# Optimization experiments

Hardware: AMD Instinct MI355X
Metric: run time of the kernel (lower is better)

The kernel has to match this reference:

```python
import jax, jax.numpy as jnp
import numpy as np

B, S, D, H = 2, 2048, 2048, 16
HD = D // H  # 128


def _rope(t, cos, sin):
    # t: [B, S, H, HD]; cos/sin: [S, HD//2]
    te, to = t[..., ::2], t[..., 1::2]
    c = cos[None, :, None, :]
    s = sin[None, :, None, :]
    re = te * c - to * s
    im = te * s + to * c
    # interleave back (matches tf.stack(..., axis=-1) + reshape)
    return jnp.stack([re, im], axis=-1).reshape(t.shape)


def setup_inputs() -> dict:
    key = jax.random.key(0)
    ks = jax.random.split(key, 6)
    x = jax.random.normal(ks[0], (B, S, D), dtype=jnp.float32)
    Wq = jax.random.normal(ks[1], (D, D), dtype=jnp.float32) * 0.02
    Wk = jax.random.normal(ks[2], (D, D), dtype=jnp.float32) * 0.02
    Wv = jax.random.normal(ks[3], (D, D), dtype=jnp.float32) * 0.02
    Wo = jax.random.normal(ks[4], (D, D), dtype=jnp.float32) * 0.02
    # rotary embeddings: freqs_cis = exp(i * pos * inv_freq)
    inv_freq = 1.0 / (10000.0 ** (jnp.arange(0, HD, 2, dtype=jnp.float32) / HD))  # [HD//2]
    angles = jnp.arange(S, dtype=jnp.float32)[:, None] * inv_freq[None, :]  # [S, HD//2]
    freqs_cos = jnp.cos(angles)
    freqs_sin = jnp.sin(angles)
    # additive causal mask [1,1,S,S]
    causal = jnp.tril(jnp.ones((S, S), dtype=bool))
    mask = jnp.where(causal, 0.0, -1e9).astype(jnp.float32)[None, None]
    return {"x": x, "Wq": Wq, "Wk": Wk, "Wv": Wv, "Wo": Wo,
            "freqs_cos": freqs_cos, "freqs_sin": freqs_sin, "mask": mask}


def reference(x, Wq, Wk, Wv, Wo, freqs_cos, freqs_sin, mask):
    b, s, d = x.shape
    xq = (x @ Wq).reshape(b, s, H, HD)
    xk = (x @ Wk).reshape(b, s, H, HD)
    xv = (x @ Wv).reshape(b, s, H, HD)
    xq = _rope(xq, freqs_cos, freqs_sin)
    xk = _rope(xk, freqs_cos, freqs_sin)
    # [B, H, S, HD]
    xq = xq.transpose(0, 2, 1, 3)
    xk = xk.transpose(0, 2, 1, 3)
    xv = xv.transpose(0, 2, 1, 3)
    scores = jnp.einsum('bhqd,bhkd->bhqk', xq, xk) / jnp.sqrt(jnp.float32(HD))
    scores = scores + mask[:, :, :s, :s]
    probs = jax.nn.softmax(scores + 1e-9, axis=-1)
    out = jnp.einsum('bhqk,bhkd->bhqd', probs, xv)
    out = out.transpose(0, 2, 1, 3).reshape(b, s, d)
    return out @ Wo
```

## Files before the change

kernel.cpp:

```cpp
#include <hip/hip_runtime.h>
#include <cstdint>

#define BB 2
#define SS 2048
#define DD 2048
#define HH 16
#define HDIM 128
#define MM (BB * SS)

typedef __attribute__((ext_vector_type(8))) short bf16x8;
typedef __attribute__((ext_vector_type(4))) short bf16x4;
typedef __attribute__((ext_vector_type(4))) float f32x4;
typedef __attribute__((ext_vector_type(16))) float f32x16;

__device__ inline short f2bf(float f) {
  union { float f; unsigned u; } v; v.f = f;
  unsigned r = v.u + 0x7FFFu + ((v.u >> 16) & 1u);
  return (short)(r >> 16);
}
__device__ inline float bf2f(short s) {
  union { float f; unsigned u; } v;
  v.u = ((unsigned)(unsigned short)s) << 16;
  return v.f;
}
__device__ inline float asf(int u) { union { int i; float f; } v; v.i = u; return v.f; }
__device__ inline int asi(float f) { union { float f; int i; } v; v.f = f; return v.i; }

__device__ inline unsigned cvtpk_bf16(float lo, float hi) {
  unsigned r;
  asm("v_cvt_pk_bf16_f32 %0, %1, %2" : "=v"(r) : "v"(lo), "v"(hi));
  return r;
}

__device__ inline void gll16(const void* g, void* l) {
  __builtin_amdgcn_global_load_lds(
      (const __attribute__((address_space(1))) void*)g,
      (__attribute__((address_space(3))) void*)l, 16, 0, 0);
}

__global__ __launch_bounds__(256) void cast_bf16_kernel(
    const float* __restrict__ x, short* __restrict__ y, int n4) {
  int i = blockIdx.x * 256 + threadIdx.x;
  if (i >= n4) return;
  float4 v = reinterpret_cast<const float4*>(x)[i];
  bf16x4 o;
  o[0] = f2bf(v.x); o[1] = f2bf(v.y); o[2] = f2bf(v.z); o[3] = f2bf(v.w);
  reinterpret_cast<bf16x4*>(y)[i] = o;
}

__global__ __launch_bounds__(256) void transpose_cast_kernel(
    const float* __restrict__ W, short* __restrict__ Wt) {
  __shared__ short tile[64][65];
  int c = threadIdx.x & 63, r4 = threadIdx.x >> 6;
  int n0 = blockIdx.x << 6, k0 = blockIdx.y << 6;
#pragma unroll
  for (int p = 0; p < 16; ++p) {
    int r = (p << 2) + r4;
    tile[c][r] = f2bf(W[(size_t)(k0 + r) * DD + n0 + c]);
  }
  __syncthreads();
#pragma unroll
  for (int p = 0; p < 16; ++p) {
    int r = (p << 2) + r4;
    Wt[(size_t)(n0 + r) * DD + k0 + c] = tile[r][c];
  }
}

__global__ __launch_bounds__(256) void qkv_gemm_kernel(
    const short* __restrict__ A, const short* __restrict__ Bt,
    short* __restrict__ Qb, short* __restrict__ Kb, short* __restrict__ Vt,
    const float* __restrict__ fc, const float* __restrict__ fs) {
  __shared__ short smem[128 * 136];
  short* As = smem;
  short* Bs = smem + 8192;
  const int tid = threadIdx.x;
  const int lane = tid & 63, w = tid >> 6;
  const int cl = lane & 15, gq = lane >> 4;
  const int wm = w >> 1, wn = w & 1;
  const int m0 = blockIdx.y << 7, n0 = blockIdx.x << 7;
  const int mat = n0 >> 11;
  f32x4 acc[4][4];
#pragma unroll
  for (int i = 0; i < 4; ++i)
#pragma unroll
    for (int j = 0; j < 4; ++j) {
      f32x4 z = {0.f, 0.f, 0.f, 0.f};
      acc[i][j] = z;
    }
  const int lrow = lane >> 3;
  const int lseg = (lane & 7) ^ lrow;

  for (int k0 = 0; k0 < DD; k0 += 64) {
#pragma unroll
    for (int i = 0; i < 4; ++i) {
      int r0 = ((w << 2) + i) << 3;
      gll16(&A[(size_t)(m0 + r0 + lrow) * DD + k0 + (lseg << 3)], &As[r0 << 6]);
      gll16(&Bt[(size_t)(n0 + r0 + lrow) * DD + k0 + (lseg << 3)], &Bs[r0 << 6]);
    }
    __syncthreads();
#pragma unroll
    for (int ks = 0; ks < 2; ++ks) {
      bf16x8 af[4], bfr[4];
#pragma unroll
      for (int f = 0; f < 4; ++f) {
        int ra = (wm << 6) + (f << 4) + cl;
        af[f] = *reinterpret_cast<const bf16x8*>(
            &As[((ra << 6) + (ks << 5) + (gq << 3)) ^ ((ra & 7) << 3)]);
        int rb = (wn << 6) + (f << 4) + cl;
        bfr[f] = *reinterpret_cast<const bf16x8*>(
            &Bs[((rb << 6) + (ks << 5) + (gq << 3)) ^ ((rb & 7) << 3)]);
      }
#pragma unroll
      for (int fm = 0; fm < 4; ++fm)
#pragma unroll
        for (int fn = 0; fn < 4; ++fn)
          acc[fm][fn] = __builtin_amdgcn_mfma_f32_16x16x32_bf16(
              af[fm], bfr[fn], acc[fm][fn], 0, 0, 0);
    }
    __syncthreads();
  }

  if (mat < 2) {
    const float qs = (mat == 0) ? 0.127517448f : 1.0f;
    short* Dst = (mat == 0) ? Qb : Kb;
#pragma unroll
    for (int fm = 0; fm < 4; ++fm)
#pragma unroll
      for (int r = 0; r < 4; ++r) {
        int mrow = m0 + (wm << 6) + (fm << 4) + (gq << 2) + r;
        int s = mrow & (SS - 1);
#pragma unroll
        for (int fn = 0; fn < 4; ++fn) {
          int c = (wn << 6) + (fn << 4) + cl;
          int i = c >> 1;
          float cv = fc[s * 64 + i], sv = fs[s * 64 + i];
          float v = acc[fm][fn][r];
          float vp = __shfl_xor(v, 1, 64);
          float out = (c & 1) ? (v * cv + vp * sv) : (v * cv - vp * sv);
          Dst[(size_t)mrow * DD + ((n0 + c) & (DD - 1))] = f2bf(out * qs);
        }
      }
  } else {
    short* Tt = smem;
#pragma unroll
    for (int fm = 0; fm < 4; ++fm)
#pragma unroll
      for (int fn = 0; fn < 4; ++fn) {
        int c = (wn << 6) + (fn << 4) + cl;
        int rb = (wm << 6) + (fm << 4) + (gq << 2);
        bf16x4 v4;
#pragma unroll
        for (int rr = 0; rr < 4; ++rr) v4[rr] = f2bf(acc[fm][fn][rr]);
        *reinterpret_cast<bf16x4*>(&Tt[c * 136 + rb]) = v4;
      }
    __syncthreads();
    int d = tid >> 1, half = tid & 1;
    int bq = m0 >> 11, s0loc = m0 & (SS - 1);
    int hv = (n0 >> 7) - 32;
    size_t vb = (((size_t)(bq * 16 + hv) * HDIM + d) * SS) + s0loc + half * 64;
#pragma unroll
    for (int j = 0; j < 8; ++j) {
      bf16x8 v = *reinterpret_cast<const bf16x8*>(&Tt[d * 136 + half * 64 + j * 8]);
      *reinterpret_cast<bf16x8*>(&Vt[vb + j * 8]) = v;
    }
  }
}

__global__ __launch_bounds__(256) void gemm_kernel(
    const short* __restrict__ A, const short* __restrict__ Bt, float* __restrict__ C,
    int Mdim, int Ndim, int Kdim) {
  __shared__ short As[128 * 64];
  __shared__ short Bs[128 * 64];
  int tid = threadIdx.x;
  int lane = tid & 63, w = tid >> 6;
  int cl = lane & 15, gq = lane >> 4;
  int wm = w >> 1, wn = w & 1;
  int m0 = blockIdx.y << 7, n0 = blockIdx.x << 7;
  f32x4 acc[4][4];
#pragma unroll
  for (int i = 0; i < 4; ++i)
#pragma unroll
    for (int j = 0; j < 4; ++j) {
      f32x4 z = {0.f, 0.f, 0.f, 0.f};
      acc[i][j] = z;
    }
  int lrow = lane >> 3;
  int lseg = (lane & 7) ^ lrow;

  for (int k0 = 0; k0 < Kdim; k0 += 64) {
#pragma unroll
    for (int i = 0; i < 4; ++i) {
      int r0 = ((w << 2) + i) << 3;
      gll16(&A[(size_t)(m0 + r0 + lrow) * Kdim + k0 + (lseg << 3)], &As[r0 << 6]);
      gll16(&Bt[(size_t)(n0 + r0 + lrow) * Kdim + k0 + (lseg << 3)], &Bs[r0 << 6]);
    }
    __syncthreads();
#pragma unroll
    for (int ks = 0; ks < 2; ++ks) {
      bf16x8 af[4], bfr[4];
#pragma unroll
      for (int f = 0; f < 4; ++f) {
        int ra = (wm << 6) + (f << 4) + cl;
        af[f] = *reinterpret_cast<const bf16x8*>(
            &As[((ra << 6) + (ks << 5) + (gq << 3)) ^ ((ra & 7) << 3)]);
        int rb = (wn << 6) + (f << 4) + cl;
        bfr[f] = *reinterpret_cast<const bf16x8*>(
            &Bs[((rb << 6) + (ks << 5) + (gq << 3)) ^ ((rb & 7) << 3)]);
      }
#pragma unroll
      for (int fm = 0; fm < 4; ++fm)
#pragma unroll
        for (int fn = 0; fn < 4; ++fn)
          acc[fm][fn] = __builtin_amdgcn_mfma_f32_16x16x32_bf16(
              af[fm], bfr[fn], acc[fm][fn], 0, 0, 0);
    }
    __syncthreads();
  }
#pragma unroll
  for (int fm = 0; fm < 4; ++fm)
#pragma unroll
    for (int r = 0; r < 4; ++r) {
      int mrow = m0 + (wm << 6) + (fm << 4) + (gq << 2) + r;
#pragma unroll
      for (int fn = 0; fn < 4; ++fn) {
        int ncol = n0 + (wn << 6) + (fn << 4) + cl;
        C[(size_t)mrow * Ndim + ncol] = acc[fm][fn][r];
      }
    }
}

__global__ __launch_bounds__(256, 2) void attn_kernel(
    const short* __restrict__ Q, const short* __restrict__ K,
    const short* __restrict__ Vt, short* __restrict__ O) {
  __shared__ short Kl[2][64 * 128];
  __shared__ short Vl[2][128 * 64];
  const int id = blockIdx.x;
  const int qi = 15 - (id >> 5);
  const int bh = id & 31;
  const int b = bh >> 4, h = bh & 15;
  const int tid = threadIdx.x;
  const int lane = tid & 63, w = tid >> 6;
  const int l31 = lane & 31, hi = lane >> 5;
  const int qw = qi * 128 + w * 32;
  const int qg = qw + l31;

  const short* Kbase = K + (size_t)b * SS * DD + h * HDIM;
  const short* Vbase = Vt + (size_t)bh * HDIM * SS;
  int krow[4], kq[4], vd[4], vs[4];
#pragma unroll
  for (int i = 0; i < 4; ++i) {
    int c = w * 4 + i;
    krow[i] = c * 4 + (lane >> 4);
    kq[i] = (lane & 15) ^ (krow[i] & 7);
    vd[i] = c * 8 + (lane >> 3);
    vs[i] = (lane & 7) ^ (vd[i] & 7);
  }

  bf16x8 qf[8];
  const size_t qoff = ((size_t)b * SS + qg) * DD + h * HDIM;
#pragma unroll
  for (int s = 0; s < 8; ++s)
    qf[s] = *reinterpret_cast<const bf16x8*>(&Q[qoff + s * 16 + hi * 8]);

  f32x16 ot[4];
#pragma unroll
  for (int dt = 0; dt < 4; ++dt)
#pragma unroll
    for (int r = 0; r < 16; ++r) ot[dt][r] = 0.f;
  float m_run = -INFINITY, l_run = 0.f;

  const int NT = 2 * qi + 2;

#pragma unroll
  for (int i = 0; i < 4; ++i) {
    gll16(Kbase + (size_t)krow[i] * DD + kq[i] * 8, &Kl[0][(w * 4 + i) * 512]);
    gll16(Vbase + (size_t)vd[i] * SS + vs[i] * 8, &Vl[0][(w * 4 + i) * 512]);
  }
  __syncthreads();

  for (int t = 0; t < NT; ++t) {
    const int cur = t & 1;
    if (t + 1 < NT) {
      const int nt64 = (t + 1) * 64;
#pragma unroll
      for (int i = 0; i < 4; ++i) {
        gll16(Kbase + (size_t)(nt64 + krow[i]) * DD + kq[i] * 8,
              &Kl[cur ^ 1][(w * 4 + i) * 512]);
        gll16(Vbase + (size_t)vd[i] * SS + nt64 + vs[i] * 8,
              &Vl[cur ^ 1][(w * 4 + i) * 512]);
      }
    }

    if (t * 64 <= qw + 31) {
      const short* Kc = Kl[cur];
      const short* Vc = Vl[cur];
      f32x16 st0, st1;
#pragma unroll
      for (int r = 0; r < 16; ++r) { st0[r] = 0.f; st1[r] = 0.f; }
      __builtin_amdgcn_s_setprio(1);
#pragma unroll
      for (int s = 0; s < 8; ++s) {
        const int cs = (s * 2 + hi);
        bf16x8 kf0 = *reinterpret_cast<const bf16x8*>(
            &Kc[l31 * 128 + ((cs ^ (l31 & 7)) << 3)]);
        st0 = __builtin_amdgcn_mfma_f32_32x32x16_bf16(kf0, qf[s], st0, 0, 0, 0);
        bf16x8 kf1 = *reinterpret_cast<const bf16x8*>(
            &Kc[(32 + l31) * 128 + ((cs ^ (l31 & 7)) << 3)]);
        st1 = __builtin_amdgcn_mfma_f32_32x32x16_bf16(kf1, qf[s], st1, 0, 0, 0);
      }
      __builtin_amdgcn_s_setprio(0);
      if (t * 64 + 63 > qw) {
#pragma unroll
        for (int r = 0; r < 16; ++r) {
          int dl = (r & 3) + 8 * (r >> 2) + 4 * hi;
          if (t * 64 + dl > qg) st0[r] = -1e30f;
          if (t * 64 + 32 + dl > qg) st1[r] = -1e30f;
        }
      }
      float mx[16];
#pragma unroll
      for (int r = 0; r < 16; ++r) mx[r] = fmaxf(st0[r], st1[r]);
#pragma unroll
      for (int off = 8; off >= 1; off >>= 1)
#pragma unroll
        for (int r = 0; r < 8; ++r)
          if (r < off) mx[r] = fmaxf(mx[r], mx[r + off]);
      float pm = mx[0];
      {
        auto sw = __builtin_amdgcn_permlane32_swap(asi(pm), asi(pm), false, false);
        pm = fmaxf(asf(sw[0]), asf(sw[1]));
      }
      if (!__all(pm <= m_run + 11.5f)) {
        float mn = fmaxf(m_run, pm);
        float al = exp2f(m_run - mn);
        m_run = mn;
        l_run *= al;
#pragma unroll
        for (int dt = 0; dt < 4; ++dt)
#pragma unroll
          for (int r = 0; r < 16; ++r) ot[dt][r] *= al;
      }
#pragma unroll
      for (int r = 0; r < 16; ++r) st0[r] = exp2f(st0[r] - m_run);
#pragma unroll
      for (int r = 0; r < 16; ++r) st1[r] = exp2f(st1[r] - m_run);
      float sm[16];
#pragma unroll
      for (int r = 0; r < 16; ++r) sm[r] = st0[r] + st1[r];
#pragma unroll
      for (int off = 8; off >= 1; off >>= 1)
#pragma unroll
        for (int r = 0; r < 8; ++r)
          if (r < off) sm[r] += sm[r + off];
      float ps = sm[0];
      {
        auto sw = __builtin_amdgcn_permlane32_swap(asi(ps), asi(ps), false, false);
        ps = asf(sw[0]) + asf(sw[1]);
      }
      l_run += ps;

      bf16x8 pf[4];
#pragma unroll
      for (int s = 0; s < 4; ++s) {
        float e0, e1, e2, e3, e4, e5, e6, e7;
        if (s < 2) {
          e0 = st0[8 * s + 0]; e1 = st0[8 * s + 1]; e2 = st0[8 * s + 2]; e3 = st0[8 * s + 3];
          e4 = st0[8 * s + 4]; e5 = st0[8 * s + 5]; e6 = st0[8 * s + 6]; e7 = st0[8 * s + 7];
        } else {
          e0 = st1[8 * (s - 2) + 0]; e1 = st1[8 * (s - 2) + 1]; e2 = st1[8 * (s - 2) + 2]; e3 = st1[8 * (s - 2) + 3];
          e4 = st1[8 * (s - 2) + 4]; e5 = st1[8 * (s - 2) + 5]; e6 = st1[8 * (s - 2) + 6]; e7 = st1[8 * (s - 2) + 7];
        }
        unsigned a0 = cvtpk_bf16(e0, e1);
        unsigned a1 = cvtpk_bf16(e2, e3);
        unsigned b0 = cvtpk_bf16(e4, e5);
        unsigned b1 = cvtpk_bf16(e6, e7);
        auto r0 = __builtin_amdgcn_permlane32_swap((int)a0, (int)b0, false, false);
        auto r1 = __builtin_amdgcn_permlane32_swap((int)a1, (int)b1, false, false);
        union { int u[4]; bf16x8 v; } pk;
        pk.u[0] = r0[0]; pk.u[1] = r1[0]; pk.u[2] = r0[1]; pk.u[3] = r1[1];
        pf[s] = pk.v;
      }

      __builtin_amdgcn_s_setprio(1);
#pragma unroll
      for (int dt = 0; dt < 4; ++dt) {
        const int vr = dt * 32 + l31;
#pragma unroll
        for (int s = 0; s < 4; ++s) {
          bf16x8 vf = *reinterpret_cast<const bf16x8*>(
              &Vc[vr * 64 + (((s * 2 + hi) ^ (vr & 7)) << 3)]);
          ot[dt] = __builtin_amdgcn_mfma_f32_32x32x16_bf16(vf, pf[s], ot[dt], 0, 0, 0);
        }
      }
      __builtin_amdgcn_s_setprio(0);
    }
    __syncthreads();
  }

  float inv = 1.0f / l_run;
  const size_t orow = ((size_t)b * SS + qg) * DD + h * HDIM;
#pragma unroll
  for (int dt = 0; dt < 4; ++dt)
#pragma unroll
    for (int g = 0; g < 4; ++g) {
      bf16x4 v;
#pragma unroll
      for (int k = 0; k < 4; ++k) v[k] = f2bf(ot[dt][4 * g + k] * inv);
      *reinterpret_cast<bf16x4*>(&O[orow + dt * 32 + 8 * g + 4 * hi]) = v;
    }
}

extern "C" void kernel_launch(void* const* d_in, const int* in_sizes, int n_in,
                              void* d_out, int out_size, void* d_ws, size_t ws_size,
                              hipStream_t stream) {
  const float* x = (const float*)d_in[0];
  const float* Wq = (const float*)d_in[1];
  const float* Wk = (const float*)d_in[2];
  const float* Wv = (const float*)d_in[3];
  const float* Wo = (const float*)d_in[4];
  const float* fc = (const float*)d_in[5];
  const float* fs = (const float*)d_in[6];
  float* out = (float*)d_out;
  char* ws = (char*)d_ws;

  short* xb     = (short*)(ws + 0);
  short* WqkvT  = (short*)(ws + (size_t)16 * 1048576);
  short* WoT    = (short*)(ws + (size_t)40 * 1048576);
  short* Qb     = (short*)(ws + (size_t)48 * 1048576);
  short* Kb     = (short*)(ws + (size_t)64 * 1048576);
  short* VtB    = (short*)(ws + (size_t)80 * 1048576);

  cast_bf16_kernel<<<8192, 256, 0, stream>>>(x, xb, 2097152);
  dim3 tg(32, 32);
  transpose_cast_kernel<<<tg, 256, 0, stream>>>(Wq, WqkvT);
  transpose_cast_kernel<<<tg, 256, 0, stream>>>(Wk, WqkvT + (size_t)2048 * 2048);
  transpose_cast_kernel<<<tg, 256, 0, stream>>>(Wv, WqkvT + (size_t)4096 * 2048);
  transpose_cast_kernel<<<tg, 256, 0, stream>>>(Wo, WoT);

  qkv_gemm_kernel<<<dim3(48, 32), 256, 0, stream>>>(xb, WqkvT, Qb, Kb, VtB, fc, fs);

  attn_kernel<<<512, 256, 0, stream>>>(Qb, Kb, VtB, xb);

  gemm_kernel<<<dim3(16, 32), 256, 0, stream>>>(xb, WoT, out, MM, DD, DD);
}
```

Measured before the change: 282.6 us.

## Use 256x256 double-buffered 8-wave QKV GEMM and transpose V separately

Replaces the 128x128 single-buffered QKV GEMM with a 256x256-tile, 512-thread kernel. It double-buffers LDS, issues next-tile loads between MFMA quarters, raises wave priority around the MFMAs, and remaps block IDs to group tiles. The V output is now written row-major and transposed by a new kernel into the freed weight buffer. This aims for more data reuse and overlap of loads with compute, at the cost of an extra launch, an extra pass over V, and 128KB of LDS per block, which limits occupancy.

```diff
diff --git a/kernel.cpp b/kernel.cpp
--- a/kernel.cpp
+++ b/kernel.cpp
@@ -66,103 +66,149 @@
   }
 }
 
-__global__ __launch_bounds__(256) void qkv_gemm_kernel(
+__global__ __launch_bounds__(256) void transpose_v_kernel(
+    const short* __restrict__ V, short* __restrict__ Vt) {
+  __shared__ short tile[64][65];
+  int c = threadIdx.x & 63, r4 = threadIdx.x >> 6;
+  int s0 = blockIdx.x << 6, d0 = blockIdx.y << 6;
+  int bh = blockIdx.z;
+  int b = bh >> 4, h = bh & 15;
+#pragma unroll
+  for (int p = 0; p < 16; ++p) {
+    int r = (p << 2) + r4;
+    tile[c][r] = V[(size_t)(b * SS + s0 + r) * DD + h * HDIM + d0 + c];
+  }
+  __syncthreads();
+#pragma unroll
+  for (int p = 0; p < 16; ++p) {
+    int r = (p << 2) + r4;
+    Vt[((size_t)bh * HDIM + d0 + r) * SS + s0 + c] = tile[r][c];
+  }
+}
+
+__global__ __launch_bounds__(512) void qkv_gemm8_kernel(
     const short* __restrict__ A, const short* __restrict__ Bt,
-    short* __restrict__ Qb, short* __restrict__ Kb, short* __restrict__ Vt,
+    short* __restrict__ Qb, short* __restrict__ Kb, short* __restrict__ Vb,
     const float* __restrict__ fc, const float* __restrict__ fs) {
-  __shared__ short smem[128 * 136];
-  short* As = smem;
-  short* Bs = smem + 8192;
+  __shared__ short smem[2][32768];
   const int tid = threadIdx.x;
   const int lane = tid & 63, w = tid >> 6;
   const int cl = lane & 15, gq = lane >> 4;
-  const int wm = w >> 1, wn = w & 1;
-  const int m0 = blockIdx.y << 7, n0 = blockIdx.x << 7;
+  const int wm = w >> 2, wn = w & 3;
+  const int bid = blockIdx.x;
+  const int wg = (bid & 7) * 48 + (bid >> 3);
+  const int tn = wg % 24, tm = wg / 24;
+  const int m0 = tm << 8, n0 = tn << 8;
   const int mat = n0 >> 11;
-  f32x4 acc[4][4];
-#pragma unroll
-  for (int i = 0; i < 4; ++i)
+
+  f32x4 acc[8][4];
+#pragma unroll
+  for (int i = 0; i < 8; ++i)
 #pragma unroll
     for (int j = 0; j < 4; ++j) {
       f32x4 z = {0.f, 0.f, 0.f, 0.f};
       acc[i][j] = z;
     }
-  const int lrow = lane >> 3;
-  const int lseg = (lane & 7) ^ lrow;
-
-  for (int k0 = 0; k0 < DD; k0 += 64) {
-#pragma unroll
-    for (int i = 0; i < 4; ++i) {
-      int r0 = ((w << 2) + i) << 3;
-      gll16(&A[(size_t)(m0 + r0 + lrow) * DD + k0 + (lseg << 3)], &As[r0 << 6]);
-      gll16(&Bt[(size_t)(n0 + r0 + lrow) * DD + k0 + (lseg << 3)], &Bs[r0 << 6]);
-    }
-    __syncthreads();
-#pragma unroll
-    for (int ks = 0; ks < 2; ++ks) {
-      bf16x8 af[4], bfr[4];
-#pragma unroll
-      for (int f = 0; f < 4; ++f) {
-        int ra = (wm << 6) + (f << 4) + cl;
-        af[f] = *reinterpret_cast<const bf16x8*>(
-            &As[((ra << 6) + (ks << 5) + (gq << 3)) ^ ((ra & 7) << 3)]);
-        int rb = (wn << 6) + (f << 4) + cl;
-        bfr[f] = *reinterpret_cast<const bf16x8*>(
-            &Bs[((rb << 6) + (ks << 5) + (gq << 3)) ^ ((rb & 7) << 3)]);
-      }
-#pragma unroll
-      for (int fm = 0; fm < 4; ++fm)
-#pragma unroll
-        for (int fn = 0; fn < 4; ++fn)
-          acc[fm][fn] = __builtin_amdgcn_mfma_f32_16x16x32_bf16(
-              af[fm], bfr[fn], acc[fm][fn], 0, 0, 0);
-    }
-    __syncthreads();
+
+  const int srow8 = lane >> 3;
+  const int sseg = lane & 7;
+
+  auto stageA = [&](int t, int j) {
+    int row = j * 64 + w * 8 + srow8;
+    int sg = sseg ^ (row & 7);
+    gll16(&A[(size_t)(m0 + row) * DD + t * 64 + sg * 8],
+          &smem[t & 1][j * 4096 + w * 512]);
+  };
+  auto stageB = [&](int t, int j) {
+    int row = j * 64 + w * 8 + srow8;
+    int sg = sseg ^ (row & 7);
+    gll16(&Bt[(size_t)(n0 + row) * DD + t * 64 + sg * 8],
+          &smem[t & 1][16384 + j * 4096 + w * 512]);
+  };
+
+#pragma unroll
+  for (int j = 0; j < 4; ++j) { stageA(0, j); stageB(0, j); }
+  asm volatile("s_waitcnt vmcnt(0)" ::: "memory");
+  __builtin_amdgcn_s_barrier();
+  __builtin_amdgcn_sched_barrier(0);
+
+  for (int t = 0; t < 32; ++t) {
+    const short* Ab = &smem[t & 1][0];
+    const short* Bb = &smem[t & 1][16384];
+#pragma unroll
+    for (int q = 0; q < 4; ++q) {
+      const int mq = q >> 1, nq = q & 1;
+      bf16x8 af[2][4], bfv[2][2];
+#pragma unroll
+      for (int ks = 0; ks < 2; ++ks) {
+#pragma unroll
+        for (int f = 0; f < 4; ++f) {
+          int ra = wm * 128 + mq * 64 + f * 16 + cl;
+          af[ks][f] = *reinterpret_cast<const bf16x8*>(
+              &Ab[(ra * 64 + ks * 32 + gq * 8) ^ ((ra & 7) << 3)]);
+        }
+#pragma unroll
+        for (int g = 0; g < 2; ++g) {
+          int rb = wn * 64 + nq * 32 + g * 16 + cl;
+          bfv[ks][g] = *reinterpret_cast<const bf16x8*>(
+              &Bb[(rb * 64 + ks * 32 + gq * 8) ^ ((rb & 7) << 3)]);
+        }
+      }
+      if (t + 1 < 32) {
+        if (q == 0) { stageA(t + 1, 0); stageA(t + 1, 1); stageB(t + 1, 0); stageB(t + 1, 1); }
+        else if (q == 1) { stageA(t + 1, 2); stageA(t + 1, 3); stageB(t + 1, 2); stageB(t + 1, 3); }
+      }
+      __builtin_amdgcn_s_barrier();
+      __builtin_amdgcn_s_setprio(1);
+#pragma unroll
+      for (int ks = 0; ks < 2; ++ks)
+#pragma unroll
+        for (int f = 0; f < 4; ++f)
+#pragma unroll
+          for (int g = 0; g < 2; ++g)
+            acc[mq * 4 + f][nq * 2 + g] = __builtin_amdgcn_mfma_f32_16x16x32_bf16(
+                af[ks][f], bfv[ks][g], acc[mq * 4 + f][nq * 2 + g], 0, 0, 0);
+      __builtin_amdgcn_s_setprio(0);
+      __builtin_amdgcn_s_barrier();
+    }
+    asm volatile("s_waitcnt vmcnt(0)" ::: "memory");
+    __builtin_amdgcn_s_barrier();
+    __builtin_amdgcn_sched_barrier(0);
   }
 
   if (mat < 2) {
     const float qs = (mat == 0) ? 0.127517448f : 1.0f;
     short* Dst = (mat == 0) ? Qb : Kb;
 #pragma unroll
-    for (int fm = 0; fm < 4; ++fm)
+    for (int fm = 0; fm < 8; ++fm)
 #pragma unroll
       for (int r = 0; r < 4; ++r) {
-        int mrow = m0 + (wm << 6) + (fm << 4) + (gq << 2) + r;
+        int mrow = m0 + wm * 128 + fm * 16 + gq * 4 + r;
         int s = mrow & (SS - 1);
 #pragma unroll
         for (int fn = 0; fn < 4; ++fn) {
-          int c = (wn << 6) + (fn << 4) + cl;
+          int ncol = n0 + wn * 64 + fn * 16 + cl;
+          int c = ncol & 127;
           int i = c >> 1;
           float cv = fc[s * 64 + i], sv = fs[s * 64 + i];
           float v = acc[fm][fn][r];
           float vp = __shfl_xor(v, 1, 64);
-          float out = (c & 1) ? (v * cv + vp * sv) : (v * cv - vp * sv);
-          Dst[(size_t)mrow * DD + ((n0 + c) & (DD - 1))] = f2bf(out * qs);
+          float o = (c & 1) ? (v * cv + vp * sv) : (v * cv - vp * sv);
+          Dst[(size_t)mrow * DD + (ncol & (DD - 1))] = f2bf(o * qs);
         }
       }
   } else {
-    short* Tt = smem;
-#pragma unroll
-    for (int fm = 0; fm < 4; ++fm)
-#pragma unroll
-      for (int fn = 0; fn < 4; ++fn) {
-        int c = (wn << 6) + (fn << 4) + cl;
-        int rb = (wm << 6) + (fm << 4) + (gq << 2);
-        bf16x4 v4;
-#pragma unroll
-        for (int rr = 0; rr < 4; ++rr) v4[rr] = f2bf(acc[fm][fn][rr]);
-        *reinterpret_cast<bf16x4*>(&Tt[c * 136 + rb]) = v4;
-      }
-    __syncthreads();
-    int d = tid >> 1, half = tid & 1;
-    int bq = m0 >> 11, s0loc = m0 & (SS - 1);
-    int hv = (n0 >> 7) - 32;
-    size_t vb = (((size_t)(bq * 16 + hv) * HDIM + d) * SS) + s0loc + half * 64;
-#pragma unroll
-    for (int j = 0; j < 8; ++j) {
-      bf16x8 v = *reinterpret_cast<const bf16x8*>(&Tt[d * 136 + half * 64 + j * 8]);
-      *reinterpret_cast<bf16x8*>(&Vt[vb + j * 8]) = v;
-    }
+#pragma unroll
+    for (int fm = 0; fm < 8; ++fm)
+#pragma unroll
+      for (int r = 0; r < 4; ++r) {
+        int mrow = m0 + wm * 128 + fm * 16 + gq * 4 + r;
+#pragma unroll
+        for (int fn = 0; fn < 4; ++fn) {
+          int ncol = n0 + wn * 64 + fn * 16 + cl;
+          Vb[(size_t)mrow * DD + (ncol - 4096)] = f2bf(acc[fm][fn][r]);
+        }
+      }
   }
 }
 
@@ -428,7 +474,8 @@
   short* WoT    = (short*)(ws + (size_t)40 * 1048576);
   short* Qb     = (short*)(ws + (size_t)48 * 1048576);
   short* Kb     = (short*)(ws + (size_t)64 * 1048576);
-  short* VtB    = (short*)(ws + (size_t)80 * 1048576);
+  short* Vb     = (short*)(ws + (size_t)80 * 1048576);
+  short* VtB    = WqkvT;
 
   cast_bf16_kernel<<<8192, 256, 0, stream>>>(x, xb, 2097152);
   dim3 tg(32, 32);
@@ -437,7 +484,9 @@
   transpose_cast_kernel<<<tg, 256, 0, stream>>>(Wv, WqkvT + (size_t)4096 * 2048);
   transpose_cast_kernel<<<tg, 256, 0, stream>>>(Wo, WoT);
 
-  qkv_gemm_kernel<<<dim3(48, 32), 256, 0, stream>>>(xb, WqkvT, Qb, Kb, VtB, fc, fs);
+  qkv_gemm8_kernel<<<384, 512, 0, stream>>>(xb, WqkvT, Qb, Kb, Vb, fc, fs);
+
+  transpose_v_kernel<<<dim3(32, 2, 32), 256, 0, stream>>>(Vb, VtB);
 
   attn_kernel<<<512, 256, 0, stream>>>(Qb, Kb, VtB, xb);
 
```

Result: slower. 294.2 us (+4.1%).
